# Kernel optimization log

Measured on AMD Instinct MI355X. Metric: run time of the kernel, lower is better.

The kernel has to match this reference:

```python
import jax, jax.numpy as jnp
import numpy as np

D_MODEL = 1024
H = 16
D_K = D_MODEL // H
D_FF = 4096
EPS = 1e-6


def setup_inputs() -> dict:
    key = jax.random.key(0)
    ks = jax.random.split(key, 12)
    B, S = 8, 1024
    s = 0.02
    inp = {
        "x": jax.random.normal(ks[0], (B, S, D_MODEL), dtype=jnp.float32),
        "src_mask": jnp.ones((B, 1, 1, S), dtype=jnp.int32),
        "wq": jax.random.normal(ks[1], (D_MODEL, D_MODEL), dtype=jnp.float32) * s,
        "bq": jnp.zeros((D_MODEL,), jnp.float32),
        "wk": jax.random.normal(ks[2], (D_MODEL, D_MODEL), dtype=jnp.float32) * s,
        "bk": jnp.zeros((D_MODEL,), jnp.float32),
        "wv": jax.random.normal(ks[3], (D_MODEL, D_MODEL), dtype=jnp.float32) * s,
        "bv": jnp.zeros((D_MODEL,), jnp.float32),
        "wo": jax.random.normal(ks[4], (D_MODEL, D_MODEL), dtype=jnp.float32) * s,
        "bo": jnp.zeros((D_MODEL,), jnp.float32),
        "w1": jax.random.normal(ks[5], (D_FF, D_MODEL), dtype=jnp.float32) * s,
        "b1": jnp.zeros((D_FF,), jnp.float32),
        "w2": jax.random.normal(ks[6], (D_MODEL, D_FF), dtype=jnp.float32) * s,
        "b2": jnp.zeros((D_MODEL,), jnp.float32),
        "ln1_a": jnp.ones((1,), jnp.float32),
        "ln1_b": jnp.zeros((1,), jnp.float32),
        "ln2_a": jnp.ones((1,), jnp.float32),
        "ln2_b": jnp.zeros((1,), jnp.float32),
    }
    return inp


def _layernorm(x, alpha, bias):
    # matches torch: std with Bessel correction (ddof=1), eps added to std
    mean = jnp.mean(x, axis=-1, keepdims=True)
    std = jnp.std(x, axis=-1, keepdims=True, ddof=1)
    return (x - mean) / (std + EPS) * alpha + bias


def reference(x, src_mask, wq, bq, wk, bk, wv, bv, wo, bo, w1, b1, w2, b2,
              ln1_a, ln1_b, ln2_a, ln2_b):
    B, S, _ = x.shape
    # --- residual 1: self attention on pre-normed x ---
    n = _layernorm(x, ln1_a, ln1_b)
    q = n @ wq.T + bq
    # NOTE: the source has a bug: key and value are views of the *query*
    # projection (w_k/w_v outputs are computed but discarded). We reproduce it.
    _ = n @ wk.T + bk
    _ = n @ wv.T + bv
    qh = q.reshape(B, S, H, D_K).transpose(0, 2, 1, 3)  # [B,H,S,dk]
    kh = qh
    vh = qh
    scores = jnp.einsum('bhqd,bhkd->bhqk', qh, kh) / jnp.sqrt(jnp.float32(D_K))
    scores = jnp.where(src_mask == 0, jnp.float32(-1e9), scores)
    attn = jax.nn.softmax(scores, axis=-1)
    ctx = jnp.einsum('bhqk,bhkd->bhqd', attn, vh)
    ctx = ctx.transpose(0, 2, 1, 3).reshape(B, S, D_MODEL)
    x = x + (ctx @ wo.T + bo)
    # --- residual 2: feed-forward (intended ReLU MLP) ---
    n2 = _layernorm(x, ln2_a, ln2_b)
    h = jax.nn.relu(n2 @ w1.T + b1)
    x = x + (h @ w2.T + b2)
    return x
```

## Files before the change

### kernel.cpp

```cpp
#include <hip/hip_runtime.h>
#include <hip/hip_bf16.h>

typedef __attribute__((ext_vector_type(8))) short short8;
typedef __attribute__((ext_vector_type(4))) float f32x4;

#define MFMA16(a, b, c) __builtin_amdgcn_mfma_f32_16x16x32_bf16((a), (b), (c), 0, 0, 0)

__device__ __forceinline__ unsigned short f2bf(float f) {
  union { float f; unsigned int u; } v; v.f = f;
  return (unsigned short)((v.u + 0x7fffu + ((v.u >> 16) & 1u)) >> 16);
}

__device__ __forceinline__ void gload_lds16(const void* g, void* l) {
  __builtin_amdgcn_global_load_lds((__attribute__((address_space(1))) void*)g,
                                   (__attribute__((address_space(3))) void*)l,
                                   16, 0, 0);
}

struct CvtArgs {
  const float* s0; const float* s1; const float* s2; const float* s3;
  unsigned short* d0; unsigned short* d1; unsigned short* d2; unsigned short* d3;
};

__global__ __launch_bounds__(256) void cvt_weights(CvtArgs a) {
  const long N0 = 1048576, N1 = 1048576, N2 = 4194304;
  long i = ((long)blockIdx.x * 256 + threadIdx.x) * 4;
  const float* s; unsigned short* d; long off;
  if (i < N0)                { s = a.s0; d = a.d0; off = i; }
  else if (i < N0 + N1)      { s = a.s1; d = a.d1; off = i - N0; }
  else if (i < N0 + N1 + N2) { s = a.s2; d = a.d2; off = i - N0 - N1; }
  else                       { s = a.s3; d = a.d3; off = i - N0 - N1 - N2; }
  float4 v = *(const float4*)(s + off);
  ushort4 o;
  o.x = f2bf(v.x); o.y = f2bf(v.y); o.z = f2bf(v.z); o.w = f2bf(v.w);
  *(ushort4*)(d + off) = o;
}

__global__ __launch_bounds__(256) void ln_kernel(
    const float* __restrict__ x,
    const float* __restrict__ alpha, const float* __restrict__ beta,
    unsigned short* __restrict__ out) {
  const int row = blockIdx.x;
  const int tid = threadIdx.x;
  const float4 v = ((const float4*)(x + (size_t)row * 1024))[tid];
  float s  = v.x + v.y + v.z + v.w;
  float sq = v.x * v.x + v.y * v.y + v.z * v.z + v.w * v.w;
  #pragma unroll
  for (int d = 32; d >= 1; d >>= 1) {
    s  += __shfl_xor(s, d, 64);
    sq += __shfl_xor(sq, d, 64);
  }
  __shared__ float red[8];
  const int w = tid >> 6;
  if ((tid & 63) == 0) { red[w] = s; red[4 + w] = sq; }
  __syncthreads();
  s  = red[0] + red[1] + red[2] + red[3];
  sq = red[4] + red[5] + red[6] + red[7];
  const float mean = s * (1.f / 1024.f);
  float var = (sq - s * mean) * (1.f / 1023.f);
  var = fmaxf(var, 0.f);
  const float rs = alpha[0] / (sqrtf(var) + 1e-6f);
  const float bb = beta[0];
  ushort4 o;
  o.x = f2bf((v.x - mean) * rs + bb);
  o.y = f2bf((v.y - mean) * rs + bb);
  o.z = f2bf((v.z - mean) * rs + bb);
  o.w = f2bf((v.w - mean) * rs + bb);
  ((ushort4*)out)[(size_t)row * 256 + tid] = o;
}

template <int OUT_BF16, int RELU, int NF>
__global__ __launch_bounds__(512, 2) void gemm2ph(
    const unsigned short* __restrict__ A, int lda,
    const unsigned short* __restrict__ B, int ldb,
    const float* __restrict__ bias,
    const float* __restrict__ residual,
    void* __restrict__ Cout,
    int M, int N, int K, int nbx) {
  __shared__ __align__(16) unsigned short lds[32768 + NF * 8192];
  const int NT = K >> 6;
  const int tid = threadIdx.x;
  const int w = tid >> 6, lane = tid & 63;
  const int cpx = gridDim.x >> 3;
  const int id = (blockIdx.x & 7) * cpx + (blockIdx.x >> 3);
  const int bx = id % nbx, by = id / nbx;
  const int row0 = by * 256, col0 = bx * (NF * 64);
  const int wr128 = (w >> 2) * 128, wcN = (w & 3) * (NF * 16);
  const int lq = lane & 15, g = lane >> 4, g4 = g * 4;
  const int strow = tid >> 3;
  const int sunit8 = ((tid & 7) ^ (strow & 7)) * 8;

  const unsigned short* Asrc = A + (size_t)(row0 + strow) * lda + sunit8;
  const unsigned short* Bsrc = B + (size_t)(col0 + strow) * ldb + sunit8;

  auto stage = [&](int buf, int tt) {
    unsigned short* Ad = lds + buf * 16384 + w * 512;
    unsigned short* Bd = lds + 32768 + buf * (NF * 4096) + w * 512;
    #pragma unroll
    for (int c = 0; c < 4; ++c)
      gload_lds16(Asrc + (size_t)(c * 64) * lda + tt * 64, Ad + c * 4096);
    #pragma unroll
    for (int c = 0; c < NF; ++c)
      gload_lds16(Bsrc + (size_t)(c * 64) * ldb + tt * 64, Bd + c * 4096);
  };

  f32x4 acc[8][NF] = {};

  stage(0, 0);
  asm volatile("s_waitcnt vmcnt(0)" ::: "memory");
  __builtin_amdgcn_s_barrier();
  int buf = 0;

  for (int t = 0; t < NT; ++t) {
    if (t + 1 < NT) stage(buf ^ 1, t + 1);
    const unsigned short* Ab = lds + buf * 16384;
    const unsigned short* Bb = lds + 32768 + buf * (NF * 4096);
    #pragma unroll
    for (int kk = 0; kk < 2; ++kk) {
      short8 af[8], bf[NF];
      #pragma unroll
      for (int m = 0; m < 8; ++m) {
        const int r = wr128 + m * 16 + lq;
        af[m] = *(const short8*)(Ab + r * 64 + (((kk * 4 + g) ^ (r & 7)) << 3));
      }
      #pragma unroll
      for (int n = 0; n < NF; ++n) {
        const int r = wcN + n * 16 + lq;
        bf[n] = *(const short8*)(Bb + r * 64 + (((kk * 4 + g) ^ (r & 7)) << 3));
      }
      __builtin_amdgcn_s_setprio(1);
      #pragma unroll
      for (int m = 0; m < 8; ++m)
        #pragma unroll
        for (int n = 0; n < NF; ++n)
          acc[m][n] = MFMA16(af[m], bf[n], acc[m][n]);
      __builtin_amdgcn_s_setprio(0);
    }
    if (t + 1 < NT) {
      asm volatile("s_waitcnt vmcnt(0)" ::: "memory");
      __builtin_amdgcn_s_barrier();
      buf ^= 1;
    }
  }

  #pragma unroll
  for (int n = 0; n < NF; ++n) {
    const int col = col0 + wcN + n * 16 + lq;
    const float bv = bias[col];
    #pragma unroll
    for (int m = 0; m < 8; ++m) {
      #pragma unroll
      for (int r = 0; r < 4; ++r) {
        const int row = row0 + wr128 + m * 16 + g4 + r;
        float v = acc[m][n][r] + bv;
        if (RELU) v = fmaxf(v, 0.f);
        const size_t idx = (size_t)row * N + col;
        if (residual) v += residual[idx];
        if (OUT_BF16) ((unsigned short*)Cout)[idx] = f2bf(v);
        else          ((float*)Cout)[idx] = v;
      }
    }
  }
}

__global__ __launch_bounds__(256) void transpose_q(
    const unsigned short* __restrict__ q, unsigned short* __restrict__ qT) {
  const int st = blockIdx.x, bh = blockIdx.y;
  const int b = bh >> 4, h = bh & 15;
  __shared__ __align__(16) unsigned short tile[64][80];
  const int tid = threadIdx.x;
  const unsigned short* src = q + ((size_t)(b * 1024 + st * 64)) * 1024 + h * 64;
  #pragma unroll
  for (int j = 0; j < 2; ++j) {
    const int u = tid + j * 256;
    const int sl = u >> 3, d8 = (u & 7) * 8;
    *(short8*)&tile[sl][d8] = *(const short8*)&src[(size_t)sl * 1024 + d8];
  }
  __syncthreads();
  unsigned short* dst = qT + ((size_t)(bh * 64)) * 1024 + st * 64;
  #pragma unroll
  for (int j = 0; j < 2; ++j) {
    const int u = tid + j * 256;
    const int dl = u >> 3, s8 = (u & 7) * 8;
    short8 o;
    #pragma unroll
    for (int i = 0; i < 8; ++i) o[i] = (short)tile[s8 + i][dl];
    *(short8*)&dst[(size_t)dl * 1024 + s8] = o;
  }
}

__global__ __launch_bounds__(256) void attn_kernel(
    const unsigned short* __restrict__ q,
    const unsigned short* __restrict__ qT,
    const int* __restrict__ mask,
    unsigned short* __restrict__ ctx) {
  __shared__ __align__(16) unsigned short Ks[2][64 * 64];
  __shared__ __align__(16) unsigned short Vs[2][64 * 64];
  __shared__ int allmask;
  const int id = blockIdx.x;
  const int bh = ((id & 7) << 4) + (id >> 6);
  const int qt = (id >> 3) & 7;
  const int b = bh >> 4, h = bh & 15;
  const int tid = threadIdx.x, w = tid >> 6, lane = tid & 63;
  const int lq = lane & 15;
  const int g = lane >> 4;
  const int lk8 = g * 8;
  const int swz = lane & 7;
  const int q0 = qt * 128 + w * 32;
  const size_t qbase = (size_t)b * (1024 * 1024) + h * 64;
  const size_t qTb = (size_t)bh * 64 * 1024;
  const int srow = lane >> 3;
  const int su = (lane & 7) ^ srow;
  const size_t ksrc = qbase + (size_t)(w * 16 + srow) * 1024 + su * 8;
  const size_t vsrc = qTb + (size_t)(w * 16 + srow) * 1024 + su * 8;
  const float SC = 0.18033688011112042f;

  auto stage = [&](int bufi, int kt) {
    char* Kd = (char*)Ks[bufi] + w * 2048;
    char* Vd = (char*)Vs[bufi] + w * 2048;
    gload_lds16(q + ksrc + (size_t)(kt * 64) * 1024, Kd);
    gload_lds16(q + ksrc + (size_t)(kt * 64 + 8) * 1024, Kd + 1024);
    gload_lds16(qT + vsrc + kt * 64, Vd);
    gload_lds16(qT + vsrc + (size_t)8 * 1024 + kt * 64, Vd + 1024);
  };

  const int* mrow = mask + b * 1024;
  if (tid == 0) allmask = 1;
  int mp = 1;
  #pragma unroll
  for (int i = 0; i < 4; ++i) mp &= (mrow[tid + i * 256] != 0);
  stage(0, 0);
  __syncthreads();
  if (!__all(mp) && lane == 0) atomicAnd(&allmask, 0);
  asm volatile("s_waitcnt vmcnt(0)" ::: "memory");
  __syncthreads();
  const bool fullmask = (allmask != 0);

  short8 qa[2][2];
  #pragma unroll
  for (int qf = 0; qf < 2; ++qf)
    #pragma unroll
    for (int kk = 0; kk < 2; ++kk)
      qa[qf][kk] = *(const short8*)&q[qbase + (size_t)(q0 + qf * 16 + lq) * 1024 + kk * 32 + lk8];

  float mrun[2] = {-1e30f, -1e30f};
  float lrun[2] = {0.f, 0.f};
  f32x4 Oa[2][4];
  #pragma unroll
  for (int mf = 0; mf < 2; ++mf)
    #pragma unroll
    for (int nf = 0; nf < 4; ++nf) Oa[mf][nf] = (f32x4){0.f, 0.f, 0.f, 0.f};

  int cur = 0;

  for (int kt = 0; kt < 16; ++kt) {
    const int k0 = kt * 64;
    if (kt < 15) stage(cur ^ 1, kt + 1);
    const char* Kb = (const char*)Ks[cur];
    const char* Vb = (const char*)Vs[cur];
    f32x4 s[2][4];
    #pragma unroll
    for (int qf = 0; qf < 2; ++qf)
      #pragma unroll
      for (int kf = 0; kf < 4; ++kf) s[qf][kf] = (f32x4){0.f, 0.f, 0.f, 0.f};
    #pragma unroll
    for (int kf = 0; kf < 4; ++kf) {
      const char* kr = Kb + (kf * 16 + lq) * 128;
      const short8 ka0 = *(const short8*)(kr + (((g) ^ swz) << 4));
      const short8 ka1 = *(const short8*)(kr + (((4 + g) ^ swz) << 4));
      s[0][kf] = MFMA16(ka0, qa[0][0], s[0][kf]);
      s[0][kf] = MFMA16(ka1, qa[0][1], s[0][kf]);
      s[1][kf] = MFMA16(ka0, qa[1][0], s[1][kf]);
      s[1][kf] = MFMA16(ka1, qa[1][1], s[1][kf]);
    }
    float pmax[2] = {-1e30f, -1e30f};
    if (fullmask) {
      #pragma unroll
      for (int kf = 0; kf < 4; ++kf)
        #pragma unroll
        for (int qf = 0; qf < 2; ++qf)
          #pragma unroll
          for (int r = 0; r < 4; ++r) {
            const float v = s[qf][kf][r] * SC;
            s[qf][kf][r] = v;
            pmax[qf] = fmaxf(pmax[qf], v);
          }
    } else {
      #pragma unroll
      for (int kf = 0; kf < 4; ++kf) {
        const int4 mv = *(const int4*)&mrow[k0 + kf * 16 + g * 4];
        float madd[4];
        madd[0] = mv.x ? 0.f : -1e9f; madd[1] = mv.y ? 0.f : -1e9f;
        madd[2] = mv.z ? 0.f : -1e9f; madd[3] = mv.w ? 0.f : -1e9f;
        #pragma unroll
        for (int qf = 0; qf < 2; ++qf)
          #pragma unroll
          for (int r = 0; r < 4; ++r) {
            const float v = s[qf][kf][r] * SC + madd[r];
            s[qf][kf][r] = v;
            pmax[qf] = fmaxf(pmax[qf], v);
          }
      }
    }
    #pragma unroll
    for (int qf = 0; qf < 2; ++qf) {
      pmax[qf] = fmaxf(pmax[qf], __shfl_xor(pmax[qf], 16, 64));
      pmax[qf] = fmaxf(pmax[qf], __shfl_xor(pmax[qf], 32, 64));
    }
    const int ok = (pmax[0] <= mrun[0] + 8.f) && (pmax[1] <= mrun[1] + 8.f);
    if (!__all(ok)) {
      float corr[2];
      #pragma unroll
      for (int qf = 0; qf < 2; ++qf) {
        const float mn = fmaxf(mrun[qf], pmax[qf]);
        corr[qf] = exp2f(mrun[qf] - mn);
        mrun[qf] = mn;
        lrun[qf] *= corr[qf];
      }
      #pragma unroll
      for (int mf = 0; mf < 2; ++mf)
        #pragma unroll
        for (int r = 0; r < 4; ++r) {
          const float c = __shfl(corr[mf], g * 4 + r, 64);
          #pragma unroll
          for (int nf = 0; nf < 4; ++nf) Oa[mf][nf][r] *= c;
        }
    }
    float tsum[2] = {0.f, 0.f};
    unsigned int E[2][4], O[2][4];
    #pragma unroll
    for (int qf = 0; qf < 2; ++qf) {
      #pragma unroll
      for (int kf = 0; kf < 4; ++kf) {
        float p0 = exp2f(s[qf][kf][0] - mrun[qf]);
        float p1 = exp2f(s[qf][kf][1] - mrun[qf]);
        float p2 = exp2f(s[qf][kf][2] - mrun[qf]);
        float p3 = exp2f(s[qf][kf][3] - mrun[qf]);
        tsum[qf] += (p0 + p1) + (p2 + p3);
        asm("v_cvt_pk_bf16_f32 %0, %1, %2" : "=v"(E[qf][kf]) : "v"(p0), "v"(p1));
        asm("v_cvt_pk_bf16_f32 %0, %1, %2" : "=v"(O[qf][kf]) : "v"(p2), "v"(p3));
      }
    }
    short8 pa[2][2];
    #pragma unroll
    for (int qf = 0; qf < 2; ++qf) {
      #pragma unroll
      for (int ks = 0; ks < 2; ++ks) {
        unsigned int e0 = E[qf][2 * ks], e1 = E[qf][2 * ks + 1];
        unsigned int o0 = O[qf][2 * ks], o1 = O[qf][2 * ks + 1];
        asm("v_permlane32_swap_b32 %0, %1" : "+v"(e0), "+v"(e1));
        asm("v_permlane16_swap_b32 %0, %1" : "+v"(e0), "+v"(e1));
        asm("v_permlane32_swap_b32 %0, %1" : "+v"(o0), "+v"(o1));
        asm("v_permlane16_swap_b32 %0, %1" : "+v"(o0), "+v"(o1));
        union { unsigned int u[4]; short8 s8; } pw;
        pw.u[0] = e0; pw.u[1] = o0; pw.u[2] = e1; pw.u[3] = o1;
        pa[qf][ks] = pw.s8;
      }
    }
    #pragma unroll
    for (int ks = 0; ks < 2; ++ks) {
      #pragma unroll
      for (int nf = 0; nf < 4; ++nf) {
        const short8 vb = *(const short8*)(Vb + (nf * 16 + lq) * 128 + (((4 * ks + g) ^ swz) << 4));
        Oa[0][nf] = MFMA16(pa[0][ks], vb, Oa[0][nf]);
        Oa[1][nf] = MFMA16(pa[1][ks], vb, Oa[1][nf]);
      }
    }
    #pragma unroll
    for (int qf = 0; qf < 2; ++qf) {
      tsum[qf] += __shfl_xor(tsum[qf], 16, 64);
      tsum[qf] += __shfl_xor(tsum[qf], 32, 64);
      lrun[qf] += tsum[qf];
    }
    __syncthreads();
    cur ^= 1;
  }
  #pragma unroll
  for (int mf = 0; mf < 2; ++mf) {
    #pragma unroll
    for (int r = 0; r < 4; ++r) {
      const float linv = 1.f / __shfl(lrun[mf], g * 4 + r, 64);
      const int row = q0 + mf * 16 + g * 4 + r;
      #pragma unroll
      for (int nf = 0; nf < 4; ++nf) {
        const int col = h * 64 + nf * 16 + lq;
        ctx[((size_t)b * 1024 + row) * 1024 + col] = f2bf(Oa[mf][nf][r] * linv);
      }
    }
  }
}

extern "C" void kernel_launch(void* const* d_in, const int* in_sizes, int n_in,
                              void* d_out, int out_size, void* d_ws, size_t ws_size,
                              hipStream_t stream) {
  const float* x    = (const float*)d_in[0];
  const int*   mask = (const int*)d_in[1];
  const float* wq   = (const float*)d_in[2];
  const float* bq   = (const float*)d_in[3];
  const float* wo   = (const float*)d_in[8];
  const float* bo   = (const float*)d_in[9];
  const float* w1   = (const float*)d_in[10];
  const float* b1   = (const float*)d_in[11];
  const float* w2   = (const float*)d_in[12];
  const float* b2   = (const float*)d_in[13];
  const float* ln1a = (const float*)d_in[14];
  const float* ln1b = (const float*)d_in[15];
  const float* ln2a = (const float*)d_in[16];
  const float* ln2b = (const float*)d_in[17];
  float* out = (float*)d_out;

  char* ws = (char*)d_ws;
  unsigned short* wq_b  = (unsigned short*)(ws);
  unsigned short* wo_b  = (unsigned short*)(ws + (2l << 20));
  unsigned short* w1_b  = (unsigned short*)(ws + (4l << 20));
  unsigned short* w2_b  = (unsigned short*)(ws + (12l << 20));
  unsigned short* n_b   = (unsigned short*)(ws + (20l << 20));
  unsigned short* q_b   = (unsigned short*)(ws + (36l << 20));
  unsigned short* qT_b  = (unsigned short*)(ws + (52l << 20));
  unsigned short* ctx_b = (unsigned short*)(ws + (68l << 20));
  unsigned short* h_b   = (unsigned short*)(ws + (84l << 20));

  CvtArgs ca{wq, wo, w1, w2, wq_b, wo_b, w1_b, w2_b};
  cvt_weights<<<10240, 256, 0, stream>>>(ca);
  ln_kernel<<<8192, 256, 0, stream>>>(x, ln1a, ln1b, n_b);
  gemm2ph<1, 0, 2><<<256, 512, 0, stream>>>(n_b, 1024, wq_b, 1024, bq, nullptr, q_b, 8192, 1024, 1024, 8);
  transpose_q<<<dim3(16, 128), 256, 0, stream>>>(q_b, qT_b);
  attn_kernel<<<1024, 256, 0, stream>>>(q_b, qT_b, mask, ctx_b);
  gemm2ph<0, 0, 2><<<256, 512, 0, stream>>>(ctx_b, 1024, wo_b, 1024, bo, x, out, 8192, 1024, 1024, 8);
  ln_kernel<<<8192, 256, 0, stream>>>(out, ln2a, ln2b, n_b);
  gemm2ph<1, 1, 4><<<512, 512, 0, stream>>>(n_b, 1024, w1_b, 1024, b1, nullptr, h_b, 8192, 4096, 1024, 16);
  gemm2ph<0, 0, 2><<<256, 512, 0, stream>>>(h_b, 4096, w2_b, 4096, b2, out, out, 8192, 1024, 4096, 8);
}
```

Before: 337.4 us.

## Fold softmax scale into Q projection, MFMA row sums, LDS-staged bf16 epilogue

The Q projection GEMM now multiplies its output by sqrt(scale·log2e). Since K and V are the same Q, the attention kernel can skip per-score scaling and rescale the output by the inverse factor at the end. Softmax row sums are now accumulated with an extra MFMA against a ones vector instead of adds and cross-lane shuffles. The bf16-output GEMM epilogue stages tiles through LDS so global writes are coalesced 16-byte stores. The tradeoff is extra MFMA work, added barriers, and a bf16 rounding change from scaling Q before quantization.

```diff
diff --git a/kernel.cpp b/kernel.cpp
--- a/kernel.cpp
+++ b/kernel.cpp
@@ -76,7 +76,7 @@
     const float* __restrict__ bias,
     const float* __restrict__ residual,
     void* __restrict__ Cout,
-    int M, int N, int K, int nbx) {
+    int M, int N, int K, float cscale, int nbx) {
   __shared__ __align__(16) unsigned short lds[32768 + NF * 8192];
   const int NT = K >> 6;
   const int tid = threadIdx.x;
@@ -143,21 +143,54 @@
     }
   }
 
-  #pragma unroll
-  for (int n = 0; n < NF; ++n) {
-    const int col = col0 + wcN + n * 16 + lq;
-    const float bv = bias[col];
-    #pragma unroll
-    for (int m = 0; m < 8; ++m) {
-      #pragma unroll
-      for (int r = 0; r < 4; ++r) {
-        const int row = row0 + wr128 + m * 16 + g4 + r;
-        float v = acc[m][n][r] + bv;
-        if (RELU) v = fmaxf(v, 0.f);
-        const size_t idx = (size_t)row * N + col;
-        if (residual) v += residual[idx];
-        if (OUT_BF16) ((unsigned short*)Cout)[idx] = f2bf(v);
-        else          ((float*)Cout)[idx] = v;
+  float bv[NF];
+  #pragma unroll
+  for (int n = 0; n < NF; ++n) bv[n] = bias[col0 + wcN + n * 16 + lq];
+
+  if (OUT_BF16) {
+    const int CW = NF * 64 + 4;
+    unsigned short* cbuf = lds;
+    __syncthreads();
+    #pragma unroll
+    for (int p = 0; p < 2; ++p) {
+      if ((w >> 2) == p) {
+        #pragma unroll
+        for (int m = 0; m < 8; ++m)
+          #pragma unroll
+          for (int n = 0; n < NF; ++n)
+            #pragma unroll
+            for (int r = 0; r < 4; ++r) {
+              float v = (acc[m][n][r] + bv[n]) * cscale;
+              if (RELU) v = fmaxf(v, 0.f);
+              cbuf[(m * 16 + g4 + r) * CW + wcN + n * 16 + lq] = f2bf(v);
+            }
+      }
+      __syncthreads();
+      #pragma unroll
+      for (int i = 0; i < 2 * NF; ++i) {
+        const int un = i * 512 + tid;
+        const int row = un / (8 * NF);
+        const int cu = un % (8 * NF);
+        const short8 vv = *(const short8*)&cbuf[row * CW + cu * 8];
+        *(short8*)((unsigned short*)Cout + (size_t)(row0 + p * 128 + row) * N + col0 + cu * 8) = vv;
+      }
+      __syncthreads();
+    }
+  } else {
+    #pragma unroll
+    for (int n = 0; n < NF; ++n) {
+      const int col = col0 + wcN + n * 16 + lq;
+      #pragma unroll
+      for (int m = 0; m < 8; ++m) {
+        #pragma unroll
+        for (int r = 0; r < 4; ++r) {
+          const int row = row0 + wr128 + m * 16 + g4 + r;
+          float v = (acc[m][n][r] + bv[n]) * cscale;
+          if (RELU) v = fmaxf(v, 0.f);
+          const size_t idx = (size_t)row * N + col;
+          if (residual) v += residual[idx];
+          ((float*)Cout)[idx] = v;
+        }
       }
     }
   }
@@ -213,7 +246,7 @@
   const int su = (lane & 7) ^ srow;
   const size_t ksrc = qbase + (size_t)(w * 16 + srow) * 1024 + su * 8;
   const size_t vsrc = qTb + (size_t)(w * 16 + srow) * 1024 + su * 8;
-  const float SC = 0.18033688011112042f;
+  const float RS = 2.3548202f;
 
   auto stage = [&](int bufi, int kt) {
     char* Kd = (char*)Ks[bufi] + w * 2048;
@@ -243,8 +276,12 @@
     for (int kk = 0; kk < 2; ++kk)
       qa[qf][kk] = *(const short8*)&q[qbase + (size_t)(q0 + qf * 16 + lq) * 1024 + kk * 32 + lk8];
 
+  short8 ones;
+  #pragma unroll
+  for (int i = 0; i < 8; ++i) ones[i] = (short)0x3F80;
+
   float mrun[2] = {-1e30f, -1e30f};
-  float lrun[2] = {0.f, 0.f};
+  f32x4 lacc[2] = {};
   f32x4 Oa[2][4];
   #pragma unroll
   for (int mf = 0; mf < 2; ++mf)
@@ -280,11 +317,8 @@
         #pragma unroll
         for (int qf = 0; qf < 2; ++qf)
           #pragma unroll
-          for (int r = 0; r < 4; ++r) {
-            const float v = s[qf][kf][r] * SC;
-            s[qf][kf][r] = v;
-            pmax[qf] = fmaxf(pmax[qf], v);
-          }
+          for (int r = 0; r < 4; ++r)
+            pmax[qf] = fmaxf(pmax[qf], s[qf][kf][r]);
     } else {
       #pragma unroll
       for (int kf = 0; kf < 4; ++kf) {
@@ -296,7 +330,7 @@
         for (int qf = 0; qf < 2; ++qf)
           #pragma unroll
           for (int r = 0; r < 4; ++r) {
-            const float v = s[qf][kf][r] * SC + madd[r];
+            const float v = s[qf][kf][r] + madd[r];
             s[qf][kf][r] = v;
             pmax[qf] = fmaxf(pmax[qf], v);
           }
@@ -315,18 +349,17 @@
         const float mn = fmaxf(mrun[qf], pmax[qf]);
         corr[qf] = exp2f(mrun[qf] - mn);
         mrun[qf] = mn;
-        lrun[qf] *= corr[qf];
       }
       #pragma unroll
       for (int mf = 0; mf < 2; ++mf)
         #pragma unroll
         for (int r = 0; r < 4; ++r) {
           const float c = __shfl(corr[mf], g * 4 + r, 64);
+          lacc[mf][r] *= c;
           #pragma unroll
           for (int nf = 0; nf < 4; ++nf) Oa[mf][nf][r] *= c;
         }
     }
-    float tsum[2] = {0.f, 0.f};
     unsigned int E[2][4], O[2][4];
     #pragma unroll
     for (int qf = 0; qf < 2; ++qf) {
@@ -336,7 +369,6 @@
         float p1 = exp2f(s[qf][kf][1] - mrun[qf]);
         float p2 = exp2f(s[qf][kf][2] - mrun[qf]);
         float p3 = exp2f(s[qf][kf][3] - mrun[qf]);
-        tsum[qf] += (p0 + p1) + (p2 + p3);
         asm("v_cvt_pk_bf16_f32 %0, %1, %2" : "=v"(E[qf][kf]) : "v"(p0), "v"(p1));
         asm("v_cvt_pk_bf16_f32 %0, %1, %2" : "=v"(O[qf][kf]) : "v"(p2), "v"(p3));
       }
@@ -365,12 +397,8 @@
         Oa[0][nf] = MFMA16(pa[0][ks], vb, Oa[0][nf]);
         Oa[1][nf] = MFMA16(pa[1][ks], vb, Oa[1][nf]);
       }
-    }
-    #pragma unroll
-    for (int qf = 0; qf < 2; ++qf) {
-      tsum[qf] += __shfl_xor(tsum[qf], 16, 64);
-      tsum[qf] += __shfl_xor(tsum[qf], 32, 64);
-      lrun[qf] += tsum[qf];
+      lacc[0] = MFMA16(pa[0][ks], ones, lacc[0]);
+      lacc[1] = MFMA16(pa[1][ks], ones, lacc[1]);
     }
     __syncthreads();
     cur ^= 1;
@@ -379,7 +407,7 @@
   for (int mf = 0; mf < 2; ++mf) {
     #pragma unroll
     for (int r = 0; r < 4; ++r) {
-      const float linv = 1.f / __shfl(lrun[mf], g * 4 + r, 64);
+      const float linv = RS / lacc[mf][r];
       const int row = q0 + mf * 16 + g * 4 + r;
       #pragma unroll
       for (int nf = 0; nf < 4; ++nf) {
@@ -420,14 +448,16 @@
   unsigned short* ctx_b = (unsigned short*)(ws + (68l << 20));
   unsigned short* h_b   = (unsigned short*)(ws + (84l << 20));
 
+  const float SQRT_SC = 0.42466090f;
+
   CvtArgs ca{wq, wo, w1, w2, wq_b, wo_b, w1_b, w2_b};
   cvt_weights<<<10240, 256, 0, stream>>>(ca);
   ln_kernel<<<8192, 256, 0, stream>>>(x, ln1a, ln1b, n_b);
-  gemm2ph<1, 0, 2><<<256, 512, 0, stream>>>(n_b, 1024, wq_b, 1024, bq, nullptr, q_b, 8192, 1024, 1024, 8);
+  gemm2ph<1, 0, 2><<<256, 512, 0, stream>>>(n_b, 1024, wq_b, 1024, bq, nullptr, q_b, 8192, 1024, 1024, SQRT_SC, 8);
   transpose_q<<<dim3(16, 128), 256, 0, stream>>>(q_b, qT_b);
   attn_kernel<<<1024, 256, 0, stream>>>(q_b, qT_b, mask, ctx_b);
-  gemm2ph<0, 0, 2><<<256, 512, 0, stream>>>(ctx_b, 1024, wo_b, 1024, bo, x, out, 8192, 1024, 1024, 8);
+  gemm2ph<0, 0, 2><<<256, 512, 0, stream>>>(ctx_b, 1024, wo_b, 1024, bo, x, out, 8192, 1024, 1024, 1.0f, 8);
   ln_kernel<<<8192, 256, 0, stream>>>(out, ln2a, ln2b, n_b);
-  gemm2ph<1, 1, 4><<<512, 512, 0, stream>>>(n_b, 1024, w1_b, 1024, b1, nullptr, h_b, 8192, 4096, 1024, 16);
-  gemm2ph<0, 0, 2><<<256, 512, 0, stream>>>(h_b, 4096, w2_b, 4096, b2, out, out, 8192, 1024, 4096, 8);
-}
+  gemm2ph<1, 1, 4><<<512, 512, 0, stream>>>(n_b, 1024, w1_b, 1024, b1, nullptr, h_b, 8192, 4096, 1024, 1.0f, 16);
+  gemm2ph<0, 0, 2><<<256, 512, 0, stream>>>(h_b, 4096, w2_b, 4096, b2, out, out, 8192, 1024, 4096, 1.0f, 8);
+}
```

Result: faster. 323.4 us (median of 2 runs) (-4.2%).
